# Performance work log

Hardware: AMD Instinct MI355X
Metric: run time of the kernel (lower is better)

The kernel has to match this reference:

```python
import jax, jax.numpy as jnp
import numpy as np

B, S, D, H = 2, 2048, 1024, 16
HD = D // H  # head depth


def setup_inputs() -> dict:
    key = jax.random.key(0)
    ks = jax.random.split(key, 8)
    scale = 0.02
    K = jax.random.normal(ks[0], (B, S, D), jnp.float32)
    V = jax.random.normal(ks[1], (B, S, D), jnp.float32)
    Q = jax.random.normal(ks[2], (B, S, D), jnp.float32)
    # causal additive mask: 1.0 where attention is disallowed (strict upper triangle)
    mask = jnp.broadcast_to(
        jnp.triu(jnp.ones((S, S), jnp.float32), k=1)[None, None, :, :], (B, 1, S, S)
    )
    Wk = jax.random.normal(ks[3], (D, D), jnp.float32) * scale
    Wv = jax.random.normal(ks[4], (D, D), jnp.float32) * scale
    Wq = jax.random.normal(ks[5], (D, D), jnp.float32) * scale
    Wo = jax.random.normal(ks[6], (D, D), jnp.float32) * scale
    z = jnp.zeros((D,), jnp.float32)
    return {"K": K, "V": V, "Q": Q, "mask": mask,
            "Wk": Wk, "bk": z, "Wv": Wv, "bv": z,
            "Wq": Wq, "bq": z, "Wo": Wo, "bo": z}


def _split_heads(x):  # [B,S,D] -> [B,H,S,HD]
    return x.reshape(B, S, H, HD).transpose(0, 2, 1, 3)


def reference(K, V, Q, mask, Wk, bk, Wv, bv, Wq, bq, Wo, bo):
    k = _split_heads(K @ Wk + bk)
    v = _split_heads(V @ Wv + bv)
    q = _split_heads(Q @ Wq + bq)
    # NOTE: source scales by sqrt(d_model), not sqrt(head_depth)
    logits = jnp.einsum("bhqd,bhkd->bhqk", q, k) / jnp.sqrt(jnp.float32(D))
    logits = logits + mask * (-1e9)
    attn = jax.nn.softmax(logits, axis=-1)
    out = jnp.einsum("bhqk,bhkd->bhqd", attn, v)  # [B,H,S,HD]
    out = out.transpose(0, 2, 1, 3).reshape(B, S, D)
    return out @ Wo + bo
```

## Files before the change

### kernel.cpp

```cpp
#include <hip/hip_runtime.h>
#include <hip/hip_bf16.h>

typedef unsigned short u16;
typedef unsigned int u32;
typedef unsigned long long u64;
typedef __attribute__((ext_vector_type(8))) __bf16 bf16x8;
typedef __attribute__((ext_vector_type(4))) float f32x4;

#define SEQ 2048
#define DM 1024
#define NH 16
#define HDim 64

__device__ __forceinline__ float bf_lo(u32 u) { return __uint_as_float(u << 16); }
__device__ __forceinline__ float bf_hi(u32 u) { return __uint_as_float(u & 0xffff0000u); }
__device__ __forceinline__ u16 f2bf(float f) {
    u32 u = __float_as_uint(f);
    u32 r = (u + 0x7fffu + ((u >> 16) & 1u)) >> 16;
    return (u16)r;
}
__device__ __forceinline__ float bf2f(u16 h) { return __uint_as_float(((u32)h) << 16); }

#define GLD16(g, l)                                                         \
    __builtin_amdgcn_global_load_lds(                                       \
        (const __attribute__((address_space(1))) void*)(g),                 \
        (__attribute__((address_space(3))) void*)(l), 16, 0, 0)

__device__ __forceinline__ bool detect_f32(const u32* q)
{
    const u32 w = q[threadIdx.x & 63];
    const int e0 = ((w & 0xffffu) >> 7) & 0xff;
    const int e1 = (w >> 23) & 0xff;
    const unsigned long long b = __ballot(e0 >= 0x90 || e1 >= 0x90);
    return b != 0ull;
}

__global__ __launch_bounds__(256)
void prep_all(const void* __restrict__ Qin, const void* __restrict__ Kin,
              const void* __restrict__ Vin,
              const void* __restrict__ w0, const void* __restrict__ w1,
              const void* __restrict__ w2, const void* __restrict__ w3,
              const void* __restrict__ b0, const void* __restrict__ b1,
              const void* __restrict__ b2, const void* __restrict__ b3,
              u16* __restrict__ Xall, u16* __restrict__ Wtall,
              u16* __restrict__ ball)
{
    __shared__ u16 T[64 * 66];
    const bool f = detect_f32((const u32*)Qin);
    const int t = threadIdx.x;
    const int bid = blockIdx.x;

    if (bid < 6144) {
        const int z = bid >> 11;
        const int bx = bid & 2047;
        const void* src = (z == 0) ? Qin : (z == 1) ? Kin : Vin;
        const size_t i0 = ((size_t)bx * 256 + t) * 8;
        u16* d = Xall + (size_t)z * 4194304 + i0;
        if (f) {
            const uint4* s = reinterpret_cast<const uint4*>((const float*)src + i0);
            uint4 a = s[0], b = s[1];
            u16 o[8];
            o[0] = f2bf(__uint_as_float(a.x)); o[1] = f2bf(__uint_as_float(a.y));
            o[2] = f2bf(__uint_as_float(a.z)); o[3] = f2bf(__uint_as_float(a.w));
            o[4] = f2bf(__uint_as_float(b.x)); o[5] = f2bf(__uint_as_float(b.y));
            o[6] = f2bf(__uint_as_float(b.z)); o[7] = f2bf(__uint_as_float(b.w));
            *reinterpret_cast<uint4*>(d) = *reinterpret_cast<const uint4*>(o);
        } else {
            *reinterpret_cast<uint4*>(d) =
                *reinterpret_cast<const uint4*>((const u16*)src + i0);
        }
    } else if (bid < 7168) {
        const int r = bid - 6144;
        const int z = r >> 8;
        const void* src = (z == 0) ? w0 : (z == 1) ? w1 : (z == 2) ? w2 : w3;
        const int n0 = ((r >> 4) & 15) * 64;
        const int k0 = (r & 15) * 64;
        const int c = t & 63, g = t >> 6;
        if (f) {
            const float* W = (const float*)src;
#pragma unroll
            for (int i = 0; i < 16; i++) {
                const int kl = g * 16 + i;
                T[kl * 66 + c] = f2bf(W[(size_t)(k0 + kl) * DM + n0 + c]);
            }
        } else {
            const u16* W = (const u16*)src;
#pragma unroll
            for (int i = 0; i < 16; i++) {
                const int kl = g * 16 + i;
                T[kl * 66 + c] = W[(size_t)(k0 + kl) * DM + n0 + c];
            }
        }
        __syncthreads();
        u16* dst = Wtall + (size_t)z * 1048576;
#pragma unroll
        for (int i = 0; i < 16; i++) {
            const int nl = g * 16 + i;
            dst[(size_t)(n0 + nl) * DM + k0 + c] = T[c * 66 + nl];
        }
    } else {
#pragma unroll
        for (int j = 0; j < 16; j++) {
            const int idx = t * 16 + j;
            const int z = idx >> 10, e = idx & 1023;
            const void* src = (z == 0) ? b0 : (z == 1) ? b1 : (z == 2) ? b2 : b3;
            ball[idx] = f ? f2bf(((const float*)src)[e]) : ((const u16*)src)[e];
        }
    }
}

__global__ __launch_bounds__(256)
void gemm128(const u16* __restrict__ Xall, const u16* __restrict__ Wtall,
             const u16* __restrict__ ball, u16* __restrict__ Yall,
             void* __restrict__ dout, int zbase, const u32* __restrict__ qdet)
{
    __shared__ __align__(16) u16 As[128 * 32];
    __shared__ __align__(16) u16 Bs[128 * 32];

    const int zz = zbase + blockIdx.z;
    const bool swp = (zz == 0) || (zz == 1);
    const u16* X  = Xall + ((zz == 3) ? 0 : (size_t)zz * 4194304);
    const u16* Wt = Wtall + (size_t)zz * 1048576;

    const int t    = threadIdx.x;
    const int w    = t >> 6;
    const int lane = t & 63;
    const int quad = lane >> 4;
    const int ln   = lane & 15;
    const int m0   = blockIdx.y * 128;
    const int n0   = blockIdx.x * 128;

    f32x4 acc[4][4];
#pragma unroll
    for (int i = 0; i < 4; i++)
#pragma unroll
        for (int j = 0; j < 4; j++) acc[i][j] = (f32x4){0.f, 0.f, 0.f, 0.f};

    const u16* ag = X  + (size_t)(m0 + w * 32 + (lane >> 2)) * DM + (lane & 3) * 8;
    const u16* bg = Wt + (size_t)(n0 + w * 32 + (lane >> 2)) * DM + (lane & 3) * 8;
    u16* al = &As[w * 1024];
    u16* bl = &Bs[w * 1024];

    const int wr = (w >> 1) * 64;
    const int wc = (w & 1) * 64;

    for (int kk = 0; kk < DM; kk += 32) {
        GLD16(ag,           al);
        GLD16(ag + 16 * DM, al + 512);
        GLD16(bg,           bl);
        GLD16(bg + 16 * DM, bl + 512);
        ag += 32; bg += 32;
        __syncthreads();

        bf16x8 af[4], bfr[4];
#pragma unroll
        for (int rt = 0; rt < 4; rt++)
            af[rt] = *reinterpret_cast<const bf16x8*>(&As[(wr + rt * 16 + ln) * 32 + quad * 8]);
#pragma unroll
        for (int ct = 0; ct < 4; ct++)
            bfr[ct] = *reinterpret_cast<const bf16x8*>(&Bs[(wc + ct * 16 + ln) * 32 + quad * 8]);
        if (swp) {
#pragma unroll
            for (int rt = 0; rt < 4; rt++)
#pragma unroll
                for (int ct = 0; ct < 4; ct++)
                    acc[rt][ct] = __builtin_amdgcn_mfma_f32_16x16x32_bf16(
                        bfr[ct], af[rt], acc[rt][ct], 0, 0, 0);
        } else {
#pragma unroll
            for (int rt = 0; rt < 4; rt++)
#pragma unroll
                for (int ct = 0; ct < 4; ct++)
                    acc[rt][ct] = __builtin_amdgcn_mfma_f32_16x16x32_bf16(
                        af[rt], bfr[ct], acc[rt][ct], 0, 0, 0);
        }
        __syncthreads();
    }

    u16* Y = Yall + (size_t)zz * 4194304;

    if (swp) {
        const float scale = (zz == 0) ? 0.03125f : 1.0f;
#pragma unroll
        for (int ct = 0; ct < 4; ct++) {
            const int nb = n0 + wc + ct * 16 + quad * 4;
            const int h = nb >> 6, hd = nb & (HDim - 1);
            float bv[4];
#pragma unroll
            for (int r = 0; r < 4; r++) bv[r] = bf2f(ball[zz * 1024 + nb + r]);
#pragma unroll
            for (int rt = 0; rt < 4; rt++) {
                const int m = m0 + wr + rt * 16 + ln;
                const int b = m >> 11, s = m & (SEQ - 1);
                u16 o4[4];
#pragma unroll
                for (int r = 0; r < 4; r++)
                    o4[r] = f2bf((acc[rt][ct][r] + bv[r]) * scale);
                *reinterpret_cast<u64*>(
                    Y + (((size_t)(b * NH + h)) * SEQ + s) * HDim + hd) =
                    *reinterpret_cast<const u64*>(o4);
            }
        }
    } else if (zz == 2) {
#pragma unroll
        for (int ct = 0; ct < 4; ct++) {
            const int n = n0 + wc + ct * 16 + ln;
            const float bv = bf2f(ball[zz * 1024 + n]);
            const int h = n >> 6, hd = n & (HDim - 1);
#pragma unroll
            for (int rt = 0; rt < 4; rt++) {
                const int m = m0 + wr + rt * 16 + quad * 4;
                const int b = m >> 11, s = m & (SEQ - 1);
                u16 o4[4];
#pragma unroll
                for (int r = 0; r < 4; r++) o4[r] = f2bf(acc[rt][ct][r] + bv);
                *reinterpret_cast<u64*>(
                    Y + (((size_t)(b * NH + h) * HDim + hd) * SEQ + s)) =
                    *reinterpret_cast<const u64*>(o4);
            }
        }
    } else {
        const bool f = detect_f32(qdet);
#pragma unroll
        for (int ct = 0; ct < 4; ct++) {
            const int n = n0 + wc + ct * 16 + ln;
            const float bv = bf2f(ball[zz * 1024 + n]);
#pragma unroll
            for (int rt = 0; rt < 4; rt++) {
                const int m = m0 + wr + rt * 16 + quad * 4;
#pragma unroll
                for (int r = 0; r < 4; r++) {
                    const float val = acc[rt][ct][r] + bv;
                    if (f) ((float*)dout)[(size_t)(m + r) * DM + n] = val;
                    else   ((u16*)dout)[(size_t)(m + r) * DM + n] = f2bf(val);
                }
            }
        }
    }
}

struct AttnAcc { f32x4 o[4]; float l[4]; };

__device__ __forceinline__ void attn_tile(
    const u16* __restrict__ Ks, const u16* __restrict__ Vs,
    u16* __restrict__ Ps, const bf16x8& qf0, const bf16x8& qf1,
    int kt, int rowb, int w, int quad, int ln, AttnAcc& a)
{
    f32x4 s[4];
#pragma unroll
    for (int ct = 0; ct < 4; ct++) {
        const u16* kr = &Ks[(ct * 16 + ln) * 72 + quad * 8];
        bf16x8 kf0 = *reinterpret_cast<const bf16x8*>(kr);
        bf16x8 kf1 = *reinterpret_cast<const bf16x8*>(kr + 32);
        f32x4 z = (f32x4){0.f, 0.f, 0.f, 0.f};
        z = __builtin_amdgcn_mfma_f32_16x16x32_bf16(qf0, kf0, z, 0, 0, 0);
        s[ct] = __builtin_amdgcn_mfma_f32_16x16x32_bf16(qf1, kf1, z, 0, 0, 0);
    }
#pragma unroll
    for (int ct = 0; ct < 4; ct++) {
        const int kcol = kt * 64 + ct * 16 + ln;
#pragma unroll
        for (int r = 0; r < 4; r++) {
            const float e = (kcol <= rowb + r) ? __expf(s[ct][r]) : 0.f;
            a.l[r] += e;
            Ps[(w * 16 + quad * 4 + r) * 68 + ct * 16 + ln] = f2bf(e);
        }
    }
#pragma unroll
    for (int ks = 0; ks < 2; ks++) {
        bf16x8 pf = *reinterpret_cast<const bf16x8*>(
            &Ps[(w * 16 + ln) * 68 + ks * 32 + quad * 8]);
#pragma unroll
        for (int nt = 0; nt < 4; nt++) {
            bf16x8 vf = *reinterpret_cast<const bf16x8*>(
                &Vs[(nt * 16 + ln) * 72 + ks * 32 + quad * 8]);
            a.o[nt] = __builtin_amdgcn_mfma_f32_16x16x32_bf16(pf, vf, a.o[nt], 0, 0, 0);
        }
    }
}

__global__ __launch_bounds__(256)
void attn_mfma(const u16* __restrict__ qh, const u16* __restrict__ kh,
               const u16* __restrict__ vt, u16* __restrict__ ctx)
{
    __shared__ __align__(16) u16 Ks[64 * 72];
    __shared__ __align__(16) u16 Vs[64 * 72];
    __shared__ __align__(16) u16 Ps[64 * 68];

    const int t    = threadIdx.x;
    const int i    = blockIdx.x;
    const int bh   = blockIdx.y;
    const int w    = t >> 6;
    const int lane = t & 63;
    const int quad = lane >> 4;
    const int ln   = lane & 15;
    const int qtH  = 31 - i;
    const int qtL  = i;

    const size_t kbase = (size_t)bh * SEQ * HDim;
    const size_t vbase = (size_t)bh * HDim * SEQ;

    const u16* qrH = qh + kbase + (size_t)(qtH * 64 + w * 16 + ln) * HDim;
    const bf16x8 qfH0 = *reinterpret_cast<const bf16x8*>(qrH + quad * 8);
    const bf16x8 qfH1 = *reinterpret_cast<const bf16x8*>(qrH + 32 + quad * 8);
    const u16* qrL = qh + kbase + (size_t)(qtL * 64 + w * 16 + ln) * HDim;
    const bf16x8 qfL0 = *reinterpret_cast<const bf16x8*>(qrL + quad * 8);
    const bf16x8 qfL1 = *reinterpret_cast<const bf16x8*>(qrL + 32 + quad * 8);

    AttnAcc aH, aL;
#pragma unroll
    for (int k = 0; k < 4; k++) {
        aH.o[k] = (f32x4){0.f, 0.f, 0.f, 0.f}; aH.l[k] = 0.f;
        aL.o[k] = (f32x4){0.f, 0.f, 0.f, 0.f}; aL.l[k] = 0.f;
    }

    const int srow = t >> 2;
    const int sc   = (t & 3) * 16;
    const int rowHb = qtH * 64 + w * 16 + quad * 4;
    const int rowLb = qtL * 64 + w * 16 + quad * 4;

    for (int kt = 0; kt <= qtH; kt++) {
        {
            const uint4* ks = reinterpret_cast<const uint4*>(
                kh + kbase + (size_t)(kt * 64 + srow) * HDim + sc);
            uint4* kd = reinterpret_cast<uint4*>(&Ks[srow * 72 + sc]);
            kd[0] = ks[0];
            kd[1] = ks[1];
            const uint4* vs = reinterpret_cast<const uint4*>(
                vt + vbase + (size_t)srow * SEQ + kt * 64 + sc);
            uint4* vd = reinterpret_cast<uint4*>(&Vs[srow * 72 + sc]);
            vd[0] = vs[0];
            vd[1] = vs[1];
        }
        __syncthreads();

        attn_tile(Ks, Vs, Ps, qfH0, qfH1, kt, rowHb, w, quad, ln, aH);
        if (kt <= qtL)
            attn_tile(Ks, Vs, Ps, qfL0, qfL1, kt, rowLb, w, quad, ln, aL);

        __syncthreads();
    }

#pragma unroll
    for (int m = 1; m < 16; m <<= 1) {
#pragma unroll
        for (int r = 0; r < 4; r++) {
            aH.l[r] += __shfl_xor(aH.l[r], m);
            aL.l[r] += __shfl_xor(aL.l[r], m);
        }
    }

    const int b = bh >> 4;
    const int h = bh & 15;
#pragma unroll
    for (int r = 0; r < 4; r++) {
        const float invH = 1.f / aH.l[r];
        const float invL = 1.f / aL.l[r];
        const int sH = qtH * 64 + w * 16 + quad * 4 + r;
        const int sL = qtL * 64 + w * 16 + quad * 4 + r;
        u16* dH = ctx + ((size_t)(b * SEQ + sH)) * DM + h * HDim + ln;
        u16* dL = ctx + ((size_t)(b * SEQ + sL)) * DM + h * HDim + ln;
#pragma unroll
        for (int nt = 0; nt < 4; nt++) {
            dH[nt * 16] = f2bf(aH.o[nt][r] * invH);
            dL[nt * 16] = f2bf(aL.o[nt][r] * invL);
        }
    }
}

__global__ __launch_bounds__(64)
void detect_dtype(const u32* __restrict__ q, int* __restrict__ flag)
{
    const int t = threadIdx.x;
    const u32 w = q[t];
    const int e0 = ((w & 0xffffu) >> 7) & 0xff;
    const int e1 = (w >> 23) & 0xff;
    const unsigned long long b = __ballot(e0 >= 0x90 || e1 >= 0x90);
    if (t == 0) *flag = (b != 0ull) ? 1 : 0;
}

__global__ __launch_bounds__(256)
void gemm_bias(const void* __restrict__ Xv, const void* __restrict__ Wv,
               const void* __restrict__ biasv, void* __restrict__ Yv,
               int M, int N, int K, int mode, int xsel, int wsel, int ysel,
               float scale, const int* __restrict__ flagp)
{
    __shared__ __align__(16) u16 As[64 * 32];
    __shared__ __align__(16) u16 Bs[64 * 40];

    const int f  = *flagp;
    const bool xf = (xsel != 0) && (f != 0);
    const bool wf = (wsel != 0) && (f != 0);
    const bool yf = (ysel != 0) && (f != 0);

    const u16*   Xb = (const u16*)Xv;
    const float* Xf = (const float*)Xv;
    const u16*   Wb = (const u16*)Wv;
    const float* Wf = (const float*)Wv;

    const int t    = threadIdx.x;
    const int m0   = blockIdx.y * 64;
    const int n0   = blockIdx.x * 64;
    const int w    = t >> 6;
    const int lane = t & 63;
    const int quad = lane >> 4;
    const int ln   = lane & 15;

    f32x4 acc[4];
#pragma unroll
    for (int i = 0; i < 4; i++) acc[i] = (f32x4){0.f, 0.f, 0.f, 0.f};

    const int a_row = t >> 2;
    const int a_c8  = (t & 3) * 8;
    const int b_n   = t & 63;
    const int b_k8  = (t >> 6) * 8;

    for (int kk = 0; kk < K; kk += 32) {
        const size_t aoff = (size_t)(m0 + a_row) * K + kk + a_c8;
        if (!xf) {
            *reinterpret_cast<uint4*>(&As[a_row * 32 + a_c8]) =
                *reinterpret_cast<const uint4*>(Xb + aoff);
        } else {
            const float* src = Xf + aoff;
            uint4 u0 = reinterpret_cast<const uint4*>(src)[0];
            uint4 u1 = reinterpret_cast<const uint4*>(src)[1];
            u16 tmp[8];
            tmp[0] = f2bf(__uint_as_float(u0.x));
            tmp[1] = f2bf(__uint_as_float(u0.y));
            tmp[2] = f2bf(__uint_as_float(u0.z));
            tmp[3] = f2bf(__uint_as_float(u0.w));
            tmp[4] = f2bf(__uint_as_float(u1.x));
            tmp[5] = f2bf(__uint_as_float(u1.y));
            tmp[6] = f2bf(__uint_as_float(u1.z));
            tmp[7] = f2bf(__uint_as_float(u1.w));
            *reinterpret_cast<uint4*>(&As[a_row * 32 + a_c8]) =
                *reinterpret_cast<const uint4*>(tmp);
        }
        u16 tmp[8];
        if (!wf) {
#pragma unroll
            for (int j = 0; j < 8; j++)
                tmp[j] = Wb[(size_t)(kk + b_k8 + j) * N + n0 + b_n];
        } else {
#pragma unroll
            for (int j = 0; j < 8; j++)
                tmp[j] = f2bf(Wf[(size_t)(kk + b_k8 + j) * N + n0 + b_n]);
        }
        *reinterpret_cast<uint4*>(&Bs[b_n * 40 + b_k8]) =
            *reinterpret_cast<const uint4*>(tmp);

        __syncthreads();

        bf16x8 bfrag = *reinterpret_cast<const bf16x8*>(&Bs[(w * 16 + ln) * 40 + quad * 8]);
#pragma unroll
        for (int rt = 0; rt < 4; rt++) {
            bf16x8 afrag = *reinterpret_cast<const bf16x8*>(&As[(rt * 16 + ln) * 32 + quad * 8]);
            acc[rt] = __builtin_amdgcn_mfma_f32_16x16x32_bf16(afrag, bfrag, acc[rt], 0, 0, 0);
        }
        __syncthreads();
    }

    const int n = n0 + w * 16 + ln;
    const float bv = wf ? ((const float*)biasv)[n] : bf2f(((const u16*)biasv)[n]);
#pragma unroll
    for (int rt = 0; rt < 4; rt++) {
        if (mode == 2) {
            const int m = m0 + rt * 16 + quad * 4;
            const int b = m >> 11;
            const int s = m & (SEQ - 1);
            const int h = n >> 6;
            const int hd = n & (HDim - 1);
            u16 o4[4];
#pragma unroll
            for (int r = 0; r < 4; r++) o4[r] = f2bf((acc[rt][r] + bv) * scale);
            *reinterpret_cast<u64*>(
                (u16*)Yv + (((size_t)(b * NH + h) * HDim + hd) * SEQ + s)) =
                *reinterpret_cast<const u64*>(o4);
        } else {
#pragma unroll
            for (int r = 0; r < 4; r++) {
                const int m = m0 + rt * 16 + quad * 4 + r;
                const float val = (acc[rt][r] + bv) * scale;
                if (mode == 0) {
                    if (yf) ((float*)Yv)[(size_t)m * N + n] = val;
                    else    ((u16*)Yv)[(size_t)m * N + n] = f2bf(val);
                } else {
                    const int b = m >> 11;
                    const int s = m & (SEQ - 1);
                    const int h = n >> 6;
                    const int hd = n & (HDim - 1);
                    ((u16*)Yv)[(((size_t)(b * NH + h)) * SEQ + s) * HDim + hd] = f2bf(val);
                }
            }
        }
    }
}

extern "C" void kernel_launch(void* const* d_in, const int* in_sizes, int n_in,
                              void* d_out, int out_size, void* d_ws, size_t ws_size,
                              hipStream_t stream)
{
    const void* Kin = d_in[0];
    const void* Vin = d_in[1];
    const void* Qin = d_in[2];
    const void* Wk = d_in[4];
    const void* bk = d_in[5];
    const void* Wv = d_in[6];
    const void* bv = d_in[7];
    const void* Wq = d_in[8];
    const void* bq = d_in[9];
    const void* Wo = d_in[10];
    const void* bo = d_in[11];

    char* ws = (char*)d_ws;
    const size_t NEED = ((size_t)29360128 + 4096) * 2 + 256;

    if (ws_size >= NEED) {
        u16* Xall  = (u16*)ws;
        u16* Yall  = (u16*)ws + 12582912;
        u16* Wtall = (u16*)ws + 25165824;
        u16* ball  = (u16*)ws + 29360128;
        u16* qhp   = Yall;
        u16* khp   = Yall + 4194304;
        u16* vtp   = Yall + 8388608;
        u16* ctx   = Xall;

        hipLaunchKernelGGL(prep_all, dim3(7169), dim3(256), 0, stream,
                           Qin, Kin, Vin, Wq, Wk, Wv, Wo, bq, bk, bv, bo,
                           Xall, Wtall, ball);

        hipLaunchKernelGGL(gemm128, dim3(8, 32, 3), dim3(256), 0, stream,
                           Xall, Wtall, ball, Yall, (void*)0, 0, (const u32*)Qin);

        hipLaunchKernelGGL(attn_mfma, dim3(16, 2 * NH), dim3(256), 0,
                           stream, qhp, khp, vtp, ctx);

        hipLaunchKernelGGL(gemm128, dim3(8, 32, 1), dim3(256), 0, stream,
                           Xall, Wtall, ball, Yall, d_out, 3, (const u32*)Qin);
    } else {
        const size_t SEG = (size_t)2 * SEQ * DM * sizeof(u16);
        u16* qh  = (u16*)(ws);
        u16* khd = (u16*)(ws + SEG);
        u16* vtd = (u16*)(ws + 2 * SEG);
        u16* ctx = (u16*)(ws + 3 * SEG);
        int* flag = (int*)(ws + 4 * SEG);

        hipLaunchKernelGGL(detect_dtype, dim3(1), dim3(64), 0, stream,
                           (const u32*)Qin, flag);

        const int M = 2 * SEQ;
        dim3 ggrid(DM / 64, M / 64);
        dim3 gblk(256);

        hipLaunchKernelGGL(gemm_bias, ggrid, gblk, 0, stream, Qin, Wq, bq, qh,  M, DM, DM, 1, 1, 1, 0, 0.03125f, flag);
        hipLaunchKernelGGL(gemm_bias, ggrid, gblk, 0, stream, Kin, Wk, bk, khd, M, DM, DM, 1, 1, 1, 0, 1.0f,     flag);
        hipLaunchKernelGGL(gemm_bias, ggrid, gblk, 0, stream, Vin, Wv, bv, vtd, M, DM, DM, 2, 1, 1, 0, 1.0f,     flag);

        hipLaunchKernelGGL(attn_mfma, dim3(16, 2 * NH), dim3(256), 0,
                           stream, qh, khd, vtd, ctx);

        hipLaunchKernelGGL(gemm_bias, ggrid, gblk, 0, stream, ctx, Wo, bo, d_out, M, DM, DM, 0, 0, 1, 1, 1.0f, flag);
    }
}
```

Before: 281.0 us.

## Split causal attention over two key ranges with a merge kernel; retile output GEMM

The attention kernel is replaced by a split version. Each query-tile pair is processed by two blocks that cover balanced halves of the causal key range. They write unnormalized bf16 partial outputs and row sums, and a new merge kernel adds the partials, normalizes, and writes the context in [B,S,D] layout. The output projection moves to a dedicated 128x64-tile GEMM, which doubles its block count. Together these aim to raise occupancy across CUs, at the cost of an extra launch, extra partial-buffer traffic, and bf16 rounding of the partials. The exponentials are taken without max subtraction, so overflow safety depends on logits staying small.

```diff
diff --git a/kernel.cpp b/kernel.cpp
--- a/kernel.cpp
+++ b/kernel.cpp
@@ -111,15 +111,14 @@
 
 __global__ __launch_bounds__(256)
 void gemm128(const u16* __restrict__ Xall, const u16* __restrict__ Wtall,
-             const u16* __restrict__ ball, u16* __restrict__ Yall,
-             void* __restrict__ dout, int zbase, const u32* __restrict__ qdet)
+             const u16* __restrict__ ball, u16* __restrict__ Yall)
 {
     __shared__ __align__(16) u16 As[128 * 32];
     __shared__ __align__(16) u16 Bs[128 * 32];
 
-    const int zz = zbase + blockIdx.z;
-    const bool swp = (zz == 0) || (zz == 1);
-    const u16* X  = Xall + ((zz == 3) ? 0 : (size_t)zz * 4194304);
+    const int zz = blockIdx.z;
+    const bool swp = (zz != 2);
+    const u16* X  = Xall + (size_t)zz * 4194304;
     const u16* Wt = Wtall + (size_t)zz * 1048576;
 
     const int t    = threadIdx.x;
@@ -201,7 +200,7 @@
                     *reinterpret_cast<const u64*>(o4);
             }
         }
-    } else if (zz == 2) {
+    } else {
 #pragma unroll
         for (int ct = 0; ct < 4; ct++) {
             const int n = n0 + wc + ct * 16 + ln;
@@ -219,24 +218,251 @@
                     *reinterpret_cast<const u64*>(o4);
             }
         }
-    } else {
-        const bool f = detect_f32(qdet);
-#pragma unroll
-        for (int ct = 0; ct < 4; ct++) {
-            const int n = n0 + wc + ct * 16 + ln;
-            const float bv = bf2f(ball[zz * 1024 + n]);
-#pragma unroll
-            for (int rt = 0; rt < 4; rt++) {
-                const int m = m0 + wr + rt * 16 + quad * 4;
-#pragma unroll
-                for (int r = 0; r < 4; r++) {
-                    const float val = acc[rt][ct][r] + bv;
-                    if (f) ((float*)dout)[(size_t)(m + r) * DM + n] = val;
-                    else   ((u16*)dout)[(size_t)(m + r) * DM + n] = f2bf(val);
-                }
+    }
+}
+
+__device__ __forceinline__ void attn_tile2(
+    const u16* __restrict__ Ks, const u16* __restrict__ Vs,
+    u16* __restrict__ Ps, const bf16x8& qf0, const bf16x8& qf1,
+    int kt, int qrow, int w, int quad, int ln, f32x4* o, float& l)
+{
+    f32x4 s[4];
+#pragma unroll
+    for (int ct = 0; ct < 4; ct++) {
+        const u16* kr = &Ks[(ct * 16 + ln) * 72 + quad * 8];
+        bf16x8 kf0 = *reinterpret_cast<const bf16x8*>(kr);
+        bf16x8 kf1 = *reinterpret_cast<const bf16x8*>(kr + 32);
+        f32x4 z = (f32x4){0.f, 0.f, 0.f, 0.f};
+        z = __builtin_amdgcn_mfma_f32_16x16x32_bf16(kf0, qf0, z, 0, 0, 0);
+        s[ct] = __builtin_amdgcn_mfma_f32_16x16x32_bf16(kf1, qf1, z, 0, 0, 0);
+    }
+#pragma unroll
+    for (int ct = 0; ct < 4; ct++) {
+        u16 o4[4];
+#pragma unroll
+        for (int r = 0; r < 4; r++) {
+            const int kcol = kt * 64 + ct * 16 + quad * 4 + r;
+            const float e = (kcol <= qrow) ? __expf(s[ct][r]) : 0.f;
+            l += e;
+            o4[r] = f2bf(e);
+        }
+        *reinterpret_cast<u64*>(&Ps[(w * 16 + ln) * 72 + ct * 16 + quad * 4]) =
+            *reinterpret_cast<const u64*>(o4);
+    }
+#pragma unroll
+    for (int ks = 0; ks < 2; ks++) {
+        bf16x8 pf = *reinterpret_cast<const bf16x8*>(
+            &Ps[(w * 16 + ln) * 72 + ks * 32 + quad * 8]);
+#pragma unroll
+        for (int nt = 0; nt < 4; nt++) {
+            bf16x8 vf = *reinterpret_cast<const bf16x8*>(
+                &Vs[(nt * 16 + ln) * 72 + ks * 32 + quad * 8]);
+            o[nt] = __builtin_amdgcn_mfma_f32_16x16x32_bf16(pf, vf, o[nt], 0, 0, 0);
+        }
+    }
+}
+
+__global__ __launch_bounds__(256)
+void attn_split(const u16* __restrict__ qh, const u16* __restrict__ kh,
+                const u16* __restrict__ vt, u16* __restrict__ Opart,
+                float* __restrict__ Lpart)
+{
+    __shared__ __align__(16) u16 Ks[64 * 72];
+    __shared__ __align__(16) u16 Vs[64 * 72];
+    __shared__ __align__(16) u16 Ps[64 * 72];
+
+    const int t    = threadIdx.x;
+    const int i    = blockIdx.x;
+    const int bh   = blockIdx.y;
+    const int c    = blockIdx.z;
+    const int w    = t >> 6;
+    const int lane = t & 63;
+    const int quad = lane >> 4;
+    const int ln   = lane & 15;
+    const int qtH  = 31 - i;
+    const int qtL  = i;
+    const int m    = (i >= 8) ? 8 : 16 - i;
+    const int kt0  = c ? m : 0;
+    const int kt1  = c ? (qtH + 1) : m;
+
+    const size_t kbase = (size_t)bh * SEQ * HDim;
+    const size_t vbase = (size_t)bh * HDim * SEQ;
+
+    const u16* qrH = qh + kbase + (size_t)(qtH * 64 + w * 16 + ln) * HDim;
+    const bf16x8 qfH0 = *reinterpret_cast<const bf16x8*>(qrH + quad * 8);
+    const bf16x8 qfH1 = *reinterpret_cast<const bf16x8*>(qrH + 32 + quad * 8);
+    const u16* qrL = qh + kbase + (size_t)(qtL * 64 + w * 16 + ln) * HDim;
+    const bf16x8 qfL0 = *reinterpret_cast<const bf16x8*>(qrL + quad * 8);
+    const bf16x8 qfL1 = *reinterpret_cast<const bf16x8*>(qrL + 32 + quad * 8);
+
+    f32x4 oH[4], oL[4];
+    float lH = 0.f, lL = 0.f;
+#pragma unroll
+    for (int k = 0; k < 4; k++) {
+        oH[k] = (f32x4){0.f, 0.f, 0.f, 0.f};
+        oL[k] = (f32x4){0.f, 0.f, 0.f, 0.f};
+    }
+
+    const int srow = t >> 2;
+    const int sc   = (t & 3) * 16;
+    const int rowH = qtH * 64 + w * 16 + ln;
+    const int rowL = qtL * 64 + w * 16 + ln;
+
+    for (int kt = kt0; kt < kt1; kt++) {
+        {
+            const uint4* ks = reinterpret_cast<const uint4*>(
+                kh + kbase + (size_t)(kt * 64 + srow) * HDim + sc);
+            uint4* kd = reinterpret_cast<uint4*>(&Ks[srow * 72 + sc]);
+            kd[0] = ks[0];
+            kd[1] = ks[1];
+            const uint4* vs = reinterpret_cast<const uint4*>(
+                vt + vbase + (size_t)srow * SEQ + kt * 64 + sc);
+            uint4* vd = reinterpret_cast<uint4*>(&Vs[srow * 72 + sc]);
+            vd[0] = vs[0];
+            vd[1] = vs[1];
+        }
+        __syncthreads();
+
+        attn_tile2(Ks, Vs, Ps, qfH0, qfH1, kt, rowH, w, quad, ln, oH, lH);
+        if (kt <= qtL)
+            attn_tile2(Ks, Vs, Ps, qfL0, qfL1, kt, rowL, w, quad, ln, oL, lL);
+
+        __syncthreads();
+    }
+
+    lH += __shfl_xor(lH, 16); lH += __shfl_xor(lH, 32);
+    lL += __shfl_xor(lL, 16); lL += __shfl_xor(lL, 32);
+
+    const size_t cb = ((size_t)c * 32 + bh) * SEQ;
+    if (lane < 16) {
+        Lpart[cb + qtH * 64 + w * 16 + lane] = lH;
+        Lpart[cb + qtL * 64 + w * 16 + lane] = lL;
+    }
+#pragma unroll
+    for (int r = 0; r < 4; r++) {
+        const int rH = qtH * 64 + w * 16 + quad * 4 + r;
+        const int rL = qtL * 64 + w * 16 + quad * 4 + r;
+        u16* dH = Opart + (cb + rH) * HDim + ln;
+        u16* dL = Opart + (cb + rL) * HDim + ln;
+#pragma unroll
+        for (int nt = 0; nt < 4; nt++) {
+            dH[nt * 16] = f2bf(oH[nt][r]);
+            dL[nt * 16] = f2bf(oL[nt][r]);
+        }
+    }
+}
+
+__global__ __launch_bounds__(256)
+void attn_merge(const u16* __restrict__ Opart, const float* __restrict__ Lpart,
+                u16* __restrict__ ctx)
+{
+    const size_t tid8 = (size_t)blockIdx.x * 256 + threadIdx.x;
+    const int d8 = (int)(tid8 & 7);
+    const int s  = (int)((tid8 >> 3) & (SEQ - 1));
+    const int bh = (int)(tid8 >> 14);
+    const size_t CSTR = (size_t)32 * SEQ * HDim;
+
+    const uint4 a = *reinterpret_cast<const uint4*>(Opart + tid8 * 8);
+    const uint4 b = *reinterpret_cast<const uint4*>(Opart + CSTR + tid8 * 8);
+    const float l0 = Lpart[(size_t)bh * SEQ + s];
+    const float l1 = Lpart[(size_t)32 * SEQ + (size_t)bh * SEQ + s];
+    const float inv = 1.f / (l0 + l1);
+
+    const u32 aw[4] = {a.x, a.y, a.z, a.w};
+    const u32 bw[4] = {b.x, b.y, b.z, b.w};
+    u32 ow[4];
+#pragma unroll
+    for (int p = 0; p < 4; p++) {
+        const float lo = (bf_lo(aw[p]) + bf_lo(bw[p])) * inv;
+        const float hi = (bf_hi(aw[p]) + bf_hi(bw[p])) * inv;
+        ow[p] = (u32)f2bf(lo) | ((u32)f2bf(hi) << 16);
+    }
+    const int bb = bh >> 4, h = bh & 15;
+    *reinterpret_cast<uint4*>(
+        ctx + ((size_t)(bb * SEQ + s)) * DM + h * HDim + d8 * 8) =
+        *reinterpret_cast<const uint4*>(ow);
+}
+
+__global__ __launch_bounds__(256)
+void gemm_out(const u16* __restrict__ ctx, const u16* __restrict__ Wt,
+              const u16* __restrict__ bias, void* __restrict__ dout,
+              const u32* __restrict__ qdet)
+{
+    __shared__ __align__(16) u16 As[128 * 32];
+    __shared__ __align__(16) u16 Bs[64 * 32];
+
+    const int t    = threadIdx.x;
+    const int w    = t >> 6;
+    const int lane = t & 63;
+    const int quad = lane >> 4;
+    const int ln   = lane & 15;
+    const int m0   = blockIdx.y * 128;
+    const int n0   = blockIdx.x * 64;
+
+    f32x4 acc[4][2];
+#pragma unroll
+    for (int i = 0; i < 4; i++)
+#pragma unroll
+        for (int j = 0; j < 2; j++) acc[i][j] = (f32x4){0.f, 0.f, 0.f, 0.f};
+
+    const u16* ag = ctx + (size_t)(m0 + w * 32 + (lane >> 2)) * DM + (lane & 3) * 8;
+    const u16* bg = Wt + (size_t)(n0 + w * 16 + (lane >> 2)) * DM + (lane & 3) * 8;
+    u16* al = &As[w * 1024];
+    u16* bl = &Bs[w * 512];
+
+    const int wr = (w >> 1) * 64;
+    const int wc = (w & 1) * 32;
+
+    for (int kk = 0; kk < DM; kk += 32) {
+        GLD16(ag,           al);
+        GLD16(ag + 16 * DM, al + 512);
+        GLD16(bg,           bl);
+        ag += 32; bg += 32;
+        __syncthreads();
+
+        bf16x8 af[4], bfr[2];
+#pragma unroll
+        for (int rt = 0; rt < 4; rt++)
+            af[rt] = *reinterpret_cast<const bf16x8*>(&As[(wr + rt * 16 + ln) * 32 + quad * 8]);
+#pragma unroll
+        for (int ct = 0; ct < 2; ct++)
+            bfr[ct] = *reinterpret_cast<const bf16x8*>(&Bs[(wc + ct * 16 + ln) * 32 + quad * 8]);
+#pragma unroll
+        for (int rt = 0; rt < 4; rt++)
+#pragma unroll
+            for (int ct = 0; ct < 2; ct++)
+                acc[rt][ct] = __builtin_amdgcn_mfma_f32_16x16x32_bf16(
+                    af[rt], bfr[ct], acc[rt][ct], 0, 0, 0);
+        __syncthreads();
+    }
+
+    const bool f = detect_f32(qdet);
+#pragma unroll
+    for (int ct = 0; ct < 2; ct++) {
+        const int n = n0 + wc + ct * 16 + ln;
+        const float bv = bf2f(bias[n]);
+#pragma unroll
+        for (int rt = 0; rt < 4; rt++) {
+            const int mb = m0 + wr + rt * 16 + quad * 4;
+#pragma unroll
+            for (int r = 0; r < 4; r++) {
+                const float val = acc[rt][ct][r] + bv;
+                if (f) ((float*)dout)[(size_t)(mb + r) * DM + n] = val;
+                else   ((u16*)dout)[(size_t)(mb + r) * DM + n] = f2bf(val);
             }
         }
     }
+}
+
+__global__ __launch_bounds__(64)
+void detect_dtype(const u32* __restrict__ q, int* __restrict__ flag)
+{
+    const int t = threadIdx.x;
+    const u32 w = q[t];
+    const int e0 = ((w & 0xffffu) >> 7) & 0xff;
+    const int e1 = (w >> 23) & 0xff;
+    const unsigned long long b = __ballot(e0 >= 0x90 || e1 >= 0x90);
+    if (t == 0) *flag = (b != 0ull) ? 1 : 0;
 }
 
 struct AttnAcc { f32x4 o[4]; float l[4]; };
@@ -366,17 +592,6 @@
             dL[nt * 16] = f2bf(aL.o[nt][r] * invL);
         }
     }
-}
-
-__global__ __launch_bounds__(64)
-void detect_dtype(const u32* __restrict__ q, int* __restrict__ flag)
-{
-    const int t = threadIdx.x;
-    const u32 w = q[t];
-    const int e0 = ((w & 0xffffu) >> 7) & 0xff;
-    const int e1 = (w >> 23) & 0xff;
-    const unsigned long long b = __ballot(e0 >= 0x90 || e1 >= 0x90);
-    if (t == 0) *flag = (b != 0ull) ? 1 : 0;
 }
 
 __global__ __launch_bounds__(256)
@@ -524,19 +739,25 @@
         u16* khp   = Yall + 4194304;
         u16* vtp   = Yall + 8388608;
         u16* ctx   = Xall;
+        u16* Opart = Xall + 4194304;
+        float* Lpart = (float*)Wtall;
 
         hipLaunchKernelGGL(prep_all, dim3(7169), dim3(256), 0, stream,
                            Qin, Kin, Vin, Wq, Wk, Wv, Wo, bq, bk, bv, bo,
                            Xall, Wtall, ball);
 
         hipLaunchKernelGGL(gemm128, dim3(8, 32, 3), dim3(256), 0, stream,
-                           Xall, Wtall, ball, Yall, (void*)0, 0, (const u32*)Qin);
-
-        hipLaunchKernelGGL(attn_mfma, dim3(16, 2 * NH), dim3(256), 0,
-                           stream, qhp, khp, vtp, ctx);
-
-        hipLaunchKernelGGL(gemm128, dim3(8, 32, 1), dim3(256), 0, stream,
-                           Xall, Wtall, ball, Yall, d_out, 3, (const u32*)Qin);
+                           Xall, Wtall, ball, Yall);
+
+        hipLaunchKernelGGL(attn_split, dim3(16, 32, 2), dim3(256), 0, stream,
+                           qhp, khp, vtp, Opart, Lpart);
+
+        hipLaunchKernelGGL(attn_merge, dim3(2048), dim3(256), 0, stream,
+                           Opart, Lpart, ctx);
+
+        hipLaunchKernelGGL(gemm_out, dim3(16, 32), dim3(256), 0, stream,
+                           ctx, Wtall + (size_t)3 * 1048576, ball + 3 * 1024,
+                           d_out, (const u32*)Qin);
     } else {
         const size_t SEG = (size_t)2 * SEQ * DM * sizeof(u16);
         u16* qh  = (u16*)(ws);
```

After: 271.8 us. 1.03x faster.
